# Optimization experiments

Hardware: AMD Instinct MI355X
Metric: run time of the kernel (lower is better)

## Reference

```python
import jax, jax.numpy as jnp
import numpy as np

B, D = 1, 128
N_STATE, N_EULER, N_FIELD = 4, 3, 1
BUF = 1  # filter_nb // 2


def setup_inputs() -> dict:
    key = jax.random.key(0)
    k1, k2, k3, k4 = jax.random.split(key, 4)
    state0 = jax.random.randint(k1, (B, D, D, D), 0, N_STATE).astype(jnp.float32)
    euler0 = jax.random.uniform(k2, (B, D, D, D, 3), dtype=jnp.float32)
    field0 = jax.random.uniform(k3, (B, D, D, D, 1), dtype=jnp.float32)
    x = jnp.concatenate([state0[..., None], euler0, field0], axis=-1)  # [B,D,D,D,5]
    out = jax.random.normal(k4, (B, D, D, D, N_STATE + N_EULER + N_FIELD), dtype=jnp.float32)
    return {"x": x, "out": out}


def _gather_neighbors(euler0):
    # euler0: [B,D,D,D,3] -> [B,D,D,D,26,3] via 26 fixed shifts (zero-padded, non-periodic)
    d = euler0.shape[1]
    pad = jnp.pad(euler0, ((0, 0), (BUF, BUF), (BUF, BUF), (BUF, BUF), (0, 0)))
    slices = []
    for di in (-1, 0, 1):
        for dj in (-1, 0, 1):
            for dk in (-1, 0, 1):
                if di == 0 and dj == 0 and dk == 0:
                    continue
                slices.append(pad[:, BUF + di:BUF + di + d,
                                  BUF + dj:BUF + dj + d,
                                  BUF + dk:BUF + dk + d, :])
    return jnp.stack(slices, axis=4)


def reference(x, out):
    # Cafe_RNN.decode with n_euler=3 (get_rot is identity).
    state0 = x[..., 0].astype(jnp.int32)                       # [B,D,D,D]
    state1 = jnp.argmax(out[..., :N_STATE], axis=-1).astype(jnp.int32)
    state1 = jnp.where(state0 == 0, 0, state1)

    field1 = out[..., -N_FIELD:]                               # [B,D,D,D,1]
    m_le1 = (state1 <= 1)[..., None]
    m_eq2 = (state1 == 2)[..., None]
    m_eq3 = (state1 == 3)[..., None]
    field1 = jnp.where(m_le1, -1.0, field1)
    field1 = jnp.where(m_eq2, jnp.clip(field1, 0.0, 0.92), field1)
    field1 = jnp.where(m_eq3, 1.0, field1)

    euler1 = x[..., 1:4]
    euler1 = jnp.where(m_le1, -1.0, euler1)

    # Solidification: for cells that just solidified, snap euler to the nearest
    # neighbor euler (min squared distance to the predicted rotation rot1).
    flag_solidify = jnp.logical_and(state0 <= 1, state1 > 1)   # [B,D,D,D]
    rot0_nbs = _gather_neighbors(x[..., 1:4])                  # [B,D,D,D,26,3]
    rot1 = out[..., N_STATE:N_STATE + N_EULER]                 # [B,D,D,D,3]
    dist = jnp.sum(jnp.square(rot0_nbs - rot1[..., None, :]), axis=-1)  # [B,D,D,D,26]
    imin = jnp.argmin(dist, axis=-1)                           # [B,D,D,D]
    chosen = jnp.take_along_axis(rot0_nbs, imin[..., None, None], axis=4)[..., 0, :]
    euler1 = jnp.where(flag_solidify[..., None], chosen, euler1)

    state1f = jax.lax.stop_gradient(state1.astype(x.dtype))
    return jnp.concatenate([state1f[..., None], euler1, field1], axis=-1)
```

## Files before the change

kernel.cpp:

```cpp
#include <hip/hip_runtime.h>

#pragma clang fp contract(off)

#define DD 128
#define NCELL (DD * DD * DD)
#define CELLS_PER_THREAD 4

__global__ __launch_bounds__(256) void cafe_rnn_kernel(
    const float* __restrict__ x,
    const float* __restrict__ out,
    float* __restrict__ y)
{
    const int t  = blockIdx.x * blockDim.x + threadIdx.x;
    const int n0 = t * CELLS_PER_THREAD;
    if (n0 >= NCELL) return;

    float4 xa[5], oa[8];
    const float4* xp = reinterpret_cast<const float4*>(x) + (size_t)t * 5;
    const float4* op = reinterpret_cast<const float4*>(out) + (size_t)t * 8;
#pragma unroll
    for (int q = 0; q < 5; ++q) xa[q] = xp[q];
#pragma unroll
    for (int q = 0; q < 8; ++q) oa[q] = op[q];

    float xv[20], ov[32], rv[20];
#pragma unroll
    for (int q = 0; q < 5; ++q) {
        xv[q * 4 + 0] = xa[q].x; xv[q * 4 + 1] = xa[q].y;
        xv[q * 4 + 2] = xa[q].z; xv[q * 4 + 3] = xa[q].w;
    }
#pragma unroll
    for (int q = 0; q < 8; ++q) {
        ov[q * 4 + 0] = oa[q].x; ov[q * 4 + 1] = oa[q].y;
        ov[q * 4 + 2] = oa[q].z; ov[q * 4 + 3] = oa[q].w;
    }

#pragma unroll
    for (int c = 0; c < CELLS_PER_THREAD; ++c) {
        const int s0 = (int)xv[c * 5 + 0];

        float b = ov[c * 8 + 0];
        int   s1 = 0;
        if (ov[c * 8 + 1] > b) { b = ov[c * 8 + 1]; s1 = 1; }
        if (ov[c * 8 + 2] > b) { b = ov[c * 8 + 2]; s1 = 2; }
        if (ov[c * 8 + 3] > b) { b = ov[c * 8 + 3]; s1 = 3; }
        if (s0 == 0) s1 = 0;

        float f1 = ov[c * 8 + 7];
        float e0 = xv[c * 5 + 1], e1 = xv[c * 5 + 2], e2 = xv[c * 5 + 3];

        if (s1 <= 1) {
            f1 = -1.0f; e0 = -1.0f; e1 = -1.0f; e2 = -1.0f;
        } else if (s1 == 2) {
            f1 = fminf(fmaxf(f1, 0.0f), 0.92f);
        } else {
            f1 = 1.0f;
        }

        if (s0 <= 1 && s1 > 1) {
            const int n = n0 + c;
            const int k = n & (DD - 1);
            const int j = (n >> 7) & (DD - 1);
            const int i = (n >> 14);
            const double r0 = (double)ov[c * 8 + 4];
            const double r1 = (double)ov[c * 8 + 5];
            const double r2 = (double)ov[c * 8 + 6];

            double best = 1.0e300;
            float ce0 = 0.0f, ce1 = 0.0f, ce2 = 0.0f;
#pragma unroll
            for (int di = -1; di <= 1; ++di) {
#pragma unroll
                for (int dj = -1; dj <= 1; ++dj) {
#pragma unroll
                    for (int dk = -1; dk <= 1; ++dk) {
                        if (di == 0 && dj == 0 && dk == 0) continue;
                        const int ii = i + di, jj = j + dj, kk = k + dk;
                        float a0 = 0.0f, a1 = 0.0f, a2 = 0.0f;
                        if ((unsigned)ii < (unsigned)DD &&
                            (unsigned)jj < (unsigned)DD &&
                            (unsigned)kk < (unsigned)DD) {
                            const float* p = x + ((size_t)((ii * DD + jj) * DD + kk)) * 5 + 1;
                            a0 = p[0]; a1 = p[1]; a2 = p[2];
                        }
                        const double d0 = (double)a0 - r0;
                        const double d1 = (double)a1 - r1;
                        const double d2 = (double)a2 - r2;
                        const double dist = d0 * d0 + d1 * d1 + d2 * d2;
                        if (dist < best) { best = dist; ce0 = a0; ce1 = a1; ce2 = a2; }
                    }
                }
            }
            e0 = ce0; e1 = ce1; e2 = ce2;
        }

        rv[c * 5 + 0] = (float)s1;
        rv[c * 5 + 1] = e0;
        rv[c * 5 + 2] = e1;
        rv[c * 5 + 3] = e2;
        rv[c * 5 + 4] = f1;
    }

    float4* yp = reinterpret_cast<float4*>(y) + (size_t)t * 5;
#pragma unroll
    for (int q = 0; q < 5; ++q) {
        float4 v;
        v.x = rv[q * 4 + 0]; v.y = rv[q * 4 + 1];
        v.z = rv[q * 4 + 2]; v.w = rv[q * 4 + 3];
        yp[q] = v;
    }
}

extern "C" void kernel_launch(void* const* d_in, const int* in_sizes, int n_in,
                              void* d_out, int out_size, void* d_ws, size_t ws_size,
                              hipStream_t stream) {
    const float* x   = (const float*)d_in[0];
    const float* out = (const float*)d_in[1];
    float* y = (float*)d_out;

    const int threads = 256;
    const int total_threads = NCELL / CELLS_PER_THREAD;
    const int blocks = total_threads / threads;
    cafe_rnn_kernel<<<blocks, threads, 0, stream>>>(x, out, y);
}
```

Measured before the change: 175.6 us.

## Split solidification neighbor search into compacted second kernel via wave ballot list

The dense pass now writes the state, euler and field outputs, and appends the indices of solidifying cells to a workspace list using a wave ballot and one atomic per wave. A second grid-stride kernel runs the 26-neighbor fp64 nearest-euler search only over the listed cells, so divergent waves no longer stall the dense streaming pass. This adds a memset, an extra launch, atomics and scattered writes, and falls back to the original single kernel when the workspace is too small.

Result: slower. 535.3 us (+204.8%).

```diff
diff --git a/kernel.cpp b/kernel.cpp
--- a/kernel.cpp
+++ b/kernel.cpp
@@ -4,15 +4,24 @@
 
 #define DD 128
 #define NCELL (DD * DD * DD)
-#define CELLS_PER_THREAD 4
-
-__global__ __launch_bounds__(256) void cafe_rnn_kernel(
+#define CPT 4
+
+__device__ __forceinline__ void nbr_off(int m, int& di, int& dj, int& dk) {
+    const int idx = (m < 13) ? m : m + 1;
+    di = idx / 9 - 1;
+    dj = (idx / 3) % 3 - 1;
+    dk = idx % 3 - 1;
+}
+
+__global__ __launch_bounds__(256) void k1_dense(
     const float* __restrict__ x,
     const float* __restrict__ out,
-    float* __restrict__ y)
+    float* __restrict__ y,
+    int* __restrict__ counter,
+    int* __restrict__ list)
 {
     const int t  = blockIdx.x * blockDim.x + threadIdx.x;
-    const int n0 = t * CELLS_PER_THREAD;
+    const int n0 = t * CPT;
     if (n0 >= NCELL) return;
 
     float4 xa[5], oa[8];
@@ -35,8 +44,10 @@
         ov[q * 4 + 2] = oa[q].z; ov[q * 4 + 3] = oa[q].w;
     }
 
-#pragma unroll
-    for (int c = 0; c < CELLS_PER_THREAD; ++c) {
+    const int lane = threadIdx.x & 63;
+
+#pragma unroll
+    for (int c = 0; c < CPT; ++c) {
         const int s0 = (int)xv[c * 5 + 0];
 
         float b = ov[c * 8 + 0];
@@ -56,6 +67,128 @@
         } else {
             f1 = 1.0f;
         }
+
+        const bool flag = (s0 <= 1 && s1 > 1);
+        const unsigned long long mask = __ballot(flag);
+        if (flag) {
+            const int lead = __ffsll(mask) - 1;
+            const unsigned long long lt = mask & ((1ull << lane) - 1ull);
+            int base = 0;
+            if (lane == lead) base = atomicAdd(counter, (int)__popcll(mask));
+            base = __shfl(base, lead, 64);
+            list[base + (int)__popcll(lt)] = n0 + c;
+        }
+
+        rv[c * 5 + 0] = (float)s1;
+        rv[c * 5 + 1] = e0;
+        rv[c * 5 + 2] = e1;
+        rv[c * 5 + 3] = e2;
+        rv[c * 5 + 4] = f1;
+    }
+
+    float4* yp = reinterpret_cast<float4*>(y) + (size_t)t * 5;
+#pragma unroll
+    for (int q = 0; q < 5; ++q) {
+        float4 v;
+        v.x = rv[q * 4 + 0]; v.y = rv[q * 4 + 1];
+        v.z = rv[q * 4 + 2]; v.w = rv[q * 4 + 3];
+        yp[q] = v;
+    }
+}
+
+__global__ __launch_bounds__(256) void k2_gather(
+    const float* __restrict__ x,
+    const float* __restrict__ out,
+    float* __restrict__ y,
+    const int* __restrict__ counter,
+    const int* __restrict__ list)
+{
+    const int cnt    = counter[0];
+    const int stride = gridDim.x * blockDim.x;
+    for (int i = blockIdx.x * blockDim.x + threadIdx.x; i < cnt; i += stride) {
+        const int n  = list[i];
+        const int k  = n & (DD - 1);
+        const int j  = (n >> 7) & (DD - 1);
+        const int i0 = n >> 14;
+
+        const float4 rot = *reinterpret_cast<const float4*>(out + (size_t)n * 8 + 4);
+        const double r0 = (double)rot.x, r1 = (double)rot.y, r2 = (double)rot.z;
+
+        float av[26][3];
+#pragma unroll
+        for (int m = 0; m < 26; ++m) {
+            int di, dj, dk;
+            nbr_off(m, di, dj, dk);
+            const int ii = i0 + di, jj = j + dj, kk = k + dk;
+            av[m][0] = 0.0f; av[m][1] = 0.0f; av[m][2] = 0.0f;
+            if ((unsigned)ii < (unsigned)DD &&
+                (unsigned)jj < (unsigned)DD &&
+                (unsigned)kk < (unsigned)DD) {
+                const float* p = x + ((size_t)((ii * DD + jj) * DD + kk)) * 5 + 1;
+                av[m][0] = p[0]; av[m][1] = p[1]; av[m][2] = p[2];
+            }
+        }
+
+        double best = 1.0e300;
+        float ce0 = 0.0f, ce1 = 0.0f, ce2 = 0.0f;
+#pragma unroll
+        for (int m = 0; m < 26; ++m) {
+            const double d0 = (double)av[m][0] - r0;
+            const double d1 = (double)av[m][1] - r1;
+            const double d2 = (double)av[m][2] - r2;
+            const double dist = d0 * d0 + d1 * d1 + d2 * d2;
+            if (dist < best) { best = dist; ce0 = av[m][0]; ce1 = av[m][1]; ce2 = av[m][2]; }
+        }
+
+        float* yp = y + (size_t)n * 5;
+        yp[1] = ce0; yp[2] = ce1; yp[3] = ce2;
+    }
+}
+
+__global__ __launch_bounds__(256) void cafe_rnn_fallback(
+    const float* __restrict__ x,
+    const float* __restrict__ out,
+    float* __restrict__ y)
+{
+    const int t  = blockIdx.x * blockDim.x + threadIdx.x;
+    const int n0 = t * CPT;
+    if (n0 >= NCELL) return;
+
+    float4 xa[5], oa[8];
+    const float4* xp = reinterpret_cast<const float4*>(x) + (size_t)t * 5;
+    const float4* op = reinterpret_cast<const float4*>(out) + (size_t)t * 8;
+#pragma unroll
+    for (int q = 0; q < 5; ++q) xa[q] = xp[q];
+#pragma unroll
+    for (int q = 0; q < 8; ++q) oa[q] = op[q];
+
+    float xv[20], ov[32], rv[20];
+#pragma unroll
+    for (int q = 0; q < 5; ++q) {
+        xv[q * 4 + 0] = xa[q].x; xv[q * 4 + 1] = xa[q].y;
+        xv[q * 4 + 2] = xa[q].z; xv[q * 4 + 3] = xa[q].w;
+    }
+#pragma unroll
+    for (int q = 0; q < 8; ++q) {
+        ov[q * 4 + 0] = oa[q].x; ov[q * 4 + 1] = oa[q].y;
+        ov[q * 4 + 2] = oa[q].z; ov[q * 4 + 3] = oa[q].w;
+    }
+
+#pragma unroll
+    for (int c = 0; c < CPT; ++c) {
+        const int s0 = (int)xv[c * 5 + 0];
+        float b = ov[c * 8 + 0];
+        int   s1 = 0;
+        if (ov[c * 8 + 1] > b) { b = ov[c * 8 + 1]; s1 = 1; }
+        if (ov[c * 8 + 2] > b) { b = ov[c * 8 + 2]; s1 = 2; }
+        if (ov[c * 8 + 3] > b) { b = ov[c * 8 + 3]; s1 = 3; }
+        if (s0 == 0) s1 = 0;
+
+        float f1 = ov[c * 8 + 7];
+        float e0 = xv[c * 5 + 1], e1 = xv[c * 5 + 2], e2 = xv[c * 5 + 3];
+        if (s1 <= 1) { f1 = -1.0f; e0 = -1.0f; e1 = -1.0f; e2 = -1.0f; }
+        else if (s1 == 2) { f1 = fminf(fmaxf(f1, 0.0f), 0.92f); }
+        else { f1 = 1.0f; }
 
         if (s0 <= 1 && s1 > 1) {
             const int n = n0 + c;
@@ -65,31 +198,25 @@
             const double r0 = (double)ov[c * 8 + 4];
             const double r1 = (double)ov[c * 8 + 5];
             const double r2 = (double)ov[c * 8 + 6];
-
             double best = 1.0e300;
             float ce0 = 0.0f, ce1 = 0.0f, ce2 = 0.0f;
 #pragma unroll
-            for (int di = -1; di <= 1; ++di) {
-#pragma unroll
-                for (int dj = -1; dj <= 1; ++dj) {
-#pragma unroll
-                    for (int dk = -1; dk <= 1; ++dk) {
-                        if (di == 0 && dj == 0 && dk == 0) continue;
-                        const int ii = i + di, jj = j + dj, kk = k + dk;
-                        float a0 = 0.0f, a1 = 0.0f, a2 = 0.0f;
-                        if ((unsigned)ii < (unsigned)DD &&
-                            (unsigned)jj < (unsigned)DD &&
-                            (unsigned)kk < (unsigned)DD) {
-                            const float* p = x + ((size_t)((ii * DD + jj) * DD + kk)) * 5 + 1;
-                            a0 = p[0]; a1 = p[1]; a2 = p[2];
-                        }
-                        const double d0 = (double)a0 - r0;
-                        const double d1 = (double)a1 - r1;
-                        const double d2 = (double)a2 - r2;
-                        const double dist = d0 * d0 + d1 * d1 + d2 * d2;
-                        if (dist < best) { best = dist; ce0 = a0; ce1 = a1; ce2 = a2; }
-                    }
+            for (int m = 0; m < 26; ++m) {
+                int di, dj, dk;
+                nbr_off(m, di, dj, dk);
+                const int ii = i + di, jj = j + dj, kk = k + dk;
+                float a0 = 0.0f, a1 = 0.0f, a2 = 0.0f;
+                if ((unsigned)ii < (unsigned)DD &&
+                    (unsigned)jj < (unsigned)DD &&
+                    (unsigned)kk < (unsigned)DD) {
+                    const float* p = x + ((size_t)((ii * DD + jj) * DD + kk)) * 5 + 1;
+                    a0 = p[0]; a1 = p[1]; a2 = p[2];
                 }
+                const double d0 = (double)a0 - r0;
+                const double d1 = (double)a1 - r1;
+                const double d2 = (double)a2 - r2;
+                const double dist = d0 * d0 + d1 * d1 + d2 * d2;
+                if (dist < best) { best = dist; ce0 = a0; ce1 = a1; ce2 = a2; }
             }
             e0 = ce0; e1 = ce1; e2 = ce2;
         }
@@ -119,7 +246,16 @@
     float* y = (float*)d_out;
 
     const int threads = 256;
-    const int total_threads = NCELL / CELLS_PER_THREAD;
-    const int blocks = total_threads / threads;
-    cafe_rnn_kernel<<<blocks, threads, 0, stream>>>(x, out, y);
-}
+    const int blocks1 = NCELL / (threads * CPT);
+
+    const size_t need = 64 + (size_t)NCELL * sizeof(int);
+    if (ws_size >= need) {
+        int* counter = (int*)d_ws;
+        int* list    = (int*)((char*)d_ws + 64);
+        hipMemsetAsync(d_ws, 0, 64, stream);
+        k1_dense<<<blocks1, threads, 0, stream>>>(x, out, y, counter, list);
+        k2_gather<<<1024, threads, 0, stream>>>(x, out, y, counter, list);
+    } else {
+        cafe_rnn_fallback<<<blocks1, threads, 0, stream>>>(x, out, y);
+    }
+}
```
